# Kernel optimization log

Measured on AMD Instinct MI355X. Metric: run time of the kernel, lower is better.

Reference implementation:

```python
import jax, jax.numpy as jnp
import numpy as np

B, S, D, H = 16, 577, 1280, 16
HD = D // H  # 80
HALF = HD // 2  # 40


def setup_inputs() -> dict:
    key = jax.random.key(0)
    ks = jax.random.split(key, 8)
    hidden_states = jax.random.normal(ks[0], (B, S, D), dtype=jnp.float32)
    # 2D rotary frequencies: random angles -> unit-magnitude complex rotations
    angles = jax.random.uniform(ks[1], (S, HALF), dtype=jnp.float32) * (2.0 * np.pi)
    freqs_cos = jnp.cos(angles)
    freqs_sin = jnp.sin(angles)
    scale = 1.0 / np.sqrt(D)
    Wq = jax.random.normal(ks[2], (D, D), dtype=jnp.float32) * scale
    Wk = jax.random.normal(ks[3], (D, D), dtype=jnp.float32) * scale
    Wv = jax.random.normal(ks[4], (D, D), dtype=jnp.float32) * scale
    Wo = jax.random.normal(ks[5], (D, D), dtype=jnp.float32) * scale
    z = jnp.zeros((D,), dtype=jnp.float32)
    return {
        "hidden_states": hidden_states,
        "freqs_cos": freqs_cos,
        "freqs_sin": freqs_sin,
        "Wq": Wq, "bq": z, "Wk": Wk, "bk": z,
        "Wv": Wv, "bv": z, "Wo": Wo, "bo": z,
    }


def _apply_rotary(x, cos, sin):
    # x: [B,S,H,HD]; cos/sin: [S, HD/2]; interleaved complex pairs (even=real, odd=imag)
    xr = x[..., 0::2]
    xi = x[..., 1::2]
    c = cos[None, :, None, :]
    s = sin[None, :, None, :]
    out_r = xr * c - xi * s
    out_i = xr * s + xi * c
    # re-interleave pairs back to [..., HD]
    return jnp.stack([out_r, out_i], axis=-1).reshape(x.shape)


def reference(hidden_states, freqs_cos, freqs_sin, Wq, bq, Wk, bk, Wv, bv, Wo, bo):
    q = (hidden_states @ Wq.T + bq).reshape(B, S, H, HD)
    k = (hidden_states @ Wk.T + bk).reshape(B, S, H, HD)
    v = (hidden_states @ Wv.T + bv).reshape(B, S, H, HD)
    q = _apply_rotary(q, freqs_cos, freqs_sin)
    k = _apply_rotary(k, freqs_cos, freqs_sin)
    # [B,H,S,HD]
    q = q.transpose(0, 2, 1, 3)
    k = k.transpose(0, 2, 1, 3)
    v = v.transpose(0, 2, 1, 3)
    scale = 1.0 / np.sqrt(HD).astype(np.float32)
    scores = jnp.einsum("bhsd,bhtd->bhst", q, k) * scale
    probs = jax.nn.softmax(scores, axis=-1)
    attn = jnp.einsum("bhst,bhtd->bhsd", probs, v)
    attn = attn.transpose(0, 2, 1, 3).reshape(B, S, D)
    return attn @ Wo.T + bo
```

## Files before the change

### kernel.cpp

```cpp
#include <hip/hip_runtime.h>

#define B_N 16
#define S_N 577
#define D_N 1280
#define H_N 16
#define HD_N 80
#define HALF_N 40
#define M_N 9232
#define M_PAD 9344
#define K_N 1280
#define VT_S 608
#define QSCALE 0.11180339887498949f

typedef __bf16 bf16_t;
typedef bf16_t bf16x8 __attribute__((ext_vector_type(8)));
typedef float f32x4 __attribute__((ext_vector_type(4)));

__device__ __forceinline__ float bf2f(unsigned short u) {
    union { unsigned int i; float f; } x; x.i = ((unsigned int)u) << 16; return x.f;
}
__device__ __forceinline__ unsigned short f2bf(float f) {
    union { unsigned int i; float f; } x; x.f = f;
    unsigned int r = x.i + 0x7FFFu + ((x.i >> 16) & 1u);
    return (unsigned short)(r >> 16);
}

__device__ __forceinline__ void gld_lds16(const unsigned short* g, unsigned short* l) {
    __builtin_amdgcn_global_load_lds(
        (const __attribute__((address_space(1))) unsigned int*)g,
        (__attribute__((address_space(3))) unsigned int*)l,
        16, 0, 0);
}

__global__ __launch_bounds__(256) void cvt_kernel(const float* __restrict__ in,
                                                  unsigned short* __restrict__ out, int n4) {
    int i = blockIdx.x * 256 + threadIdx.x;
    if (i < n4) {
        float4 v = ((const float4*)in)[i];
        ushort4 o;
        o.x = f2bf(v.x); o.y = f2bf(v.y); o.z = f2bf(v.z); o.w = f2bf(v.w);
        ((ushort4*)out)[i] = o;
    }
}

#define W4_N (D_N * K_N / 4)
__global__ __launch_bounds__(256) void cvt4_kernel(
    const float* __restrict__ w0, const float* __restrict__ w1,
    const float* __restrict__ w2, const float* __restrict__ w3,
    unsigned short* __restrict__ out) {
    int i = blockIdx.x * 256 + threadIdx.x;
    if (i >= 4 * W4_N) return;
    int r = i / W4_N, j = i - r * W4_N;
    const float* src = (r == 0) ? w0 : (r == 1) ? w1 : (r == 2) ? w2 : w3;
    float4 v = ((const float4*)src)[j];
    ushort4 o;
    o.x = f2bf(v.x); o.y = f2bf(v.y); o.z = f2bf(v.z); o.w = f2bf(v.w);
    ((ushort4*)out)[i] = o;
}

__global__ __launch_bounds__(256) void qkv32_kernel(
    const unsigned short* __restrict__ A,
    const unsigned short* __restrict__ Wb,
    const float* __restrict__ b0, const float* __restrict__ b1,
    const float* __restrict__ b2,
    const float* __restrict__ cosb, const float* __restrict__ sinb,
    void* __restrict__ o0, void* __restrict__ o1, void* __restrict__ o2)
{
    __shared__ __align__(16) unsigned short As[4][128 * 32];
    __shared__ __align__(16) unsigned short Bs[4][128 * 32];

    const int tid = threadIdx.x;
    const int wave = tid >> 6, lane = tid & 63;
    const int quad = lane >> 4, n = lane & 15;
    const int wm = wave >> 1, wn = wave & 1;
    const int m0 = blockIdx.y * 128, n0g = blockIdx.x * 128;

    const int scb = (lane & 3) ^ ((lane >> 3) & 3);

    const unsigned short* gA = A + (size_t)(m0 + wave * 32 + (lane >> 2)) * K_N + scb * 8;
    const unsigned short* gB = Wb + (size_t)(n0g + wave * 32 + (lane >> 2)) * K_N + scb * 8;

    f32x4 acc[4][4] = {};

    auto stage = [&](int s, int kt) {
        unsigned short* lA = &As[s][wave * 1024];
        unsigned short* lB = &Bs[s][wave * 1024];
        const unsigned short* a = gA + kt * 32;
        const unsigned short* b = gB + kt * 32;
        gld_lds16(a, lA);
        gld_lds16(a + 16 * K_N, lA + 512);
        gld_lds16(b, lB);
        gld_lds16(b + 16 * K_N, lB + 512);
    };

    const int sa_blk = (quad ^ ((n >> 1) & 3)) * 8;
    auto compute = [&](int s) {
        bf16x8 af[4], bfr[4];
        #pragma unroll
        for (int nt = 0; nt < 4; ++nt)
            bfr[nt] = *(const bf16x8*)&Bs[s][(wn * 64 + nt * 16 + n) * 32 + sa_blk];
        #pragma unroll
        for (int mt = 0; mt < 4; ++mt)
            af[mt] = *(const bf16x8*)&As[s][(wm * 64 + mt * 16 + n) * 32 + sa_blk];
        #pragma unroll
        for (int mt = 0; mt < 4; ++mt)
            #pragma unroll
            for (int nt = 0; nt < 4; ++nt)
                acc[mt][nt] = __builtin_amdgcn_mfma_f32_16x16x32_bf16(
                    af[mt], bfr[nt], acc[mt][nt], 0, 0, 0);
    };

    stage(0, 0); stage(1, 1); stage(2, 2);

    #pragma unroll 4
    for (int t = 0; t < 40; ++t) {
        const int tn = (t + 3 < 40) ? t + 3 : 39;
        stage((t + 3) & 3, tn);
        asm volatile("s_waitcnt vmcnt(12)" ::: "memory");
        __builtin_amdgcn_s_barrier();
        compute(t & 3);
        __builtin_amdgcn_s_barrier();
    }
    asm volatile("s_waitcnt vmcnt(0)" ::: "memory");

    const int mbase = m0 + wm * 64;
    const int wsel = blockIdx.x / 10;
    const float* bias = (wsel == 0) ? b0 : (wsel == 1) ? b1 : b2;
    unsigned short* out =
        (unsigned short*)((wsel == 0) ? o0 : (wsel == 1) ? o1 : o2);
    const int nloc = n0g - wsel * 1280 + wn * 64;
    const bool evn = (n & 1) == 0;
    #pragma unroll
    for (int nt = 0; nt < 4; ++nt) {
        const int ncol = nloc + nt * 16 + n;
        const int h = ncol / HD_N, hd = ncol - h * HD_N;
        const float bv = bias[ncol];
        #pragma unroll
        for (int mt = 0; mt < 4; ++mt)
            #pragma unroll
            for (int r = 0; r < 4; ++r) {
                int mrow = mbase + mt * 16 + quad * 4 + r;
                int b = mrow / S_N, s = mrow - b * S_N;
                float v = acc[mt][nt][r] + bv;
                if (wsel == 2) {
                    if (mrow < M_N)
                        out[((size_t)(b * H_N + h) * HD_N + hd) * VT_S + s] = f2bf(v);
                } else {
                    float pv = __shfl_xor(v, 1);
                    float c  = cosb[s * HALF_N + (hd >> 1)];
                    float sn = sinb[s * HALF_N + (hd >> 1)];
                    float res = evn ? (v * c - pv * sn) : (pv * sn + v * c);
                    if (wsel == 0) res *= QSCALE;
                    if (mrow < M_N)
                        out[((size_t)(b * H_N + h) * S_N + s) * HD_N + hd] = f2bf(res);
                }
            }
    }
}

__global__ __launch_bounds__(256) void mgemm64_kernel(
    const unsigned short* __restrict__ A,
    const unsigned short* __restrict__ Wb,
    const float* __restrict__ b0,
    void* __restrict__ o0)
{
    __shared__ __align__(16) unsigned short As[2][128 * 64];
    __shared__ __align__(16) unsigned short Bs[2][128 * 64];

    const int tid = threadIdx.x;
    const int wave = tid >> 6, lane = tid & 63;
    const int quad = lane >> 4, n = lane & 15;
    const int wm = wave >> 1, wn = wave & 1;
    const int m0 = blockIdx.y * 128, n0g = blockIdx.x * 128;

    const int srow = lane >> 3;
    const int scol = (((lane & 7) ^ srow) * 8);

    const unsigned short* gA = A + (size_t)(m0 + wave * 32 + srow) * K_N + scol;
    const unsigned short* gB = Wb + (size_t)(n0g + wave * 32 + srow) * K_N + scol;
    const int lofs = wave * 32 * 64;

    f32x4 acc[4][4] = {};

    auto stage = [&](int pp, int k0) {
        unsigned short* lA = &As[pp][lofs];
        unsigned short* lB = &Bs[pp][lofs];
        #pragma unroll
        for (int i = 0; i < 4; ++i) {
            gld_lds16(gA + k0 + i * 8 * K_N, lA + i * 512);
            gld_lds16(gB + k0 + i * 8 * K_N, lB + i * 512);
        }
    };

    auto compute = [&](int pp) {
        #pragma unroll
        for (int kk = 0; kk < 2; ++kk) {
            const int sa = ((((kk << 2) | quad) ^ (n & 7)) * 8);
            bf16x8 af[4], bfr[4];
            #pragma unroll
            for (int mt = 0; mt < 4; ++mt)
                af[mt] = *(const bf16x8*)&As[pp][(wm * 64 + mt * 16 + n) * 64 + sa];
            #pragma unroll
            for (int nt = 0; nt < 4; ++nt)
                bfr[nt] = *(const bf16x8*)&Bs[pp][(wn * 64 + nt * 16 + n) * 64 + sa];
            #pragma unroll
            for (int mt = 0; mt < 4; ++mt)
                #pragma unroll
                for (int nt = 0; nt < 4; ++nt)
                    acc[mt][nt] = __builtin_amdgcn_mfma_f32_16x16x32_bf16(
                        af[mt], bfr[nt], acc[mt][nt], 0, 0, 0);
        }
    };

    stage(0, 0);

    #pragma unroll 2
    for (int t = 0; t < 19; ++t) {
        const int pp = t & 1;
        stage(pp ^ 1, (t + 1) * 64);
        asm volatile("s_waitcnt vmcnt(8)" ::: "memory");
        __builtin_amdgcn_s_barrier();
        compute(pp);
        __builtin_amdgcn_s_barrier();
    }
    asm volatile("s_waitcnt vmcnt(0)" ::: "memory");
    __builtin_amdgcn_s_barrier();
    compute(1);

    const int mbase = m0 + wm * 64;
    const int nbase = n0g + wn * 64;
    float* outp = (float*)o0;
    #pragma unroll
    for (int mt = 0; mt < 4; ++mt)
        #pragma unroll
        for (int nt = 0; nt < 4; ++nt) {
            const int ncol = nbase + nt * 16 + n;
            const float bv = b0[ncol];
            #pragma unroll
            for (int r = 0; r < 4; ++r) {
                int mrow = mbase + mt * 16 + quad * 4 + r;
                if (mrow < M_N)
                    outp[(size_t)mrow * D_N + ncol] = acc[mt][nt][r] + bv;
            }
        }
}

__global__ __launch_bounds__(256) void fattn_kernel(
    const unsigned short* __restrict__ qb,
    const unsigned short* __restrict__ kb,
    const unsigned short* __restrict__ vt,
    unsigned short* __restrict__ attn)
{
    __shared__ __align__(16) unsigned short Plds[4][2][2][16 * 32];

    const int tid = threadIdx.x;
    const int wave = tid >> 6, lane = tid & 63;
    const int quad = lane >> 4, n = lane & 15;

    const int bid = blockIdx.x;
    const int xcd = bid & 7, t = bid >> 3;
    const int qt = t % 5, hl = t / 5;
    const int bh = hl * 8 + xcd;
    const int q0 = qt * 128 + wave * 32;

    const bf16x8 zf{};
    const unsigned short* qrow0 = qb + ((size_t)bh * S_N + q0 + n) * HD_N;
    const unsigned short* qrow1 = qrow0 + 16 * HD_N;
    bf16x8 aq00 = *(const bf16x8*)(qrow0 + quad * 8);
    bf16x8 aq01 = *(const bf16x8*)(qrow0 + 32 + quad * 8);
    bf16x8 aq02 = (quad < 2) ? *(const bf16x8*)(qrow0 + 64 + quad * 8) : zf;
    bf16x8 aq10 = *(const bf16x8*)(qrow1 + quad * 8);
    bf16x8 aq11 = *(const bf16x8*)(qrow1 + 32 + quad * 8);
    bf16x8 aq12 = (quad < 2) ? *(const bf16x8*)(qrow1 + 64 + quad * 8) : zf;

    const bf16_t one = (bf16_t)1.0f;
    const bf16x8 vones_all = {one, one, one, one, one, one, one, one};
    const bf16x8 vones = (n == 0) ? vones_all : zf;

    f32x4 o0[6] = {};
    f32x4 o1[6] = {};

    const unsigned short* kbase = kb + (size_t)bh * S_N * HD_N;
    const unsigned short* vbase = vt + (size_t)bh * HD_N * VT_S;

    #pragma unroll 2
    for (int t0 = 0; t0 < 608; t0 += 32) {
        const int pp = (t0 >> 5) & 1;
        unsigned short* pl0 = &Plds[wave][pp][0][0];
        unsigned short* pl1 = &Plds[wave][pp][1][0];

        const unsigned short* krA = kbase + (size_t)(t0 + n) * HD_N;
        const unsigned short* krB = krA + 16 * HD_N;
        bf16x8 bA0 = *(const bf16x8*)(krA + quad * 8);
        bf16x8 bA1 = *(const bf16x8*)(krA + 32 + quad * 8);
        bf16x8 bA2 = (quad < 2) ? *(const bf16x8*)(krA + 64 + quad * 8) : zf;
        bf16x8 bB0 = *(const bf16x8*)(krB + quad * 8);
        bf16x8 bB1 = *(const bf16x8*)(krB + 32 + quad * 8);
        bf16x8 bB2 = (quad < 2) ? *(const bf16x8*)(krB + 64 + quad * 8) : zf;

        f32x4 c00{}, c01{}, c10{}, c11{};
        c00 = __builtin_amdgcn_mfma_f32_16x16x32_bf16(aq00, bA0, c00, 0, 0, 0);
        c00 = __builtin_amdgcn_mfma_f32_16x16x32_bf16(aq01, bA1, c00, 0, 0, 0);
        c00 = __builtin_amdgcn_mfma_f32_16x16x32_bf16(aq02, bA2, c00, 0, 0, 0);
        c01 = __builtin_amdgcn_mfma_f32_16x16x32_bf16(aq00, bB0, c01, 0, 0, 0);
        c01 = __builtin_amdgcn_mfma_f32_16x16x32_bf16(aq01, bB1, c01, 0, 0, 0);
        c01 = __builtin_amdgcn_mfma_f32_16x16x32_bf16(aq02, bB2, c01, 0, 0, 0);
        c10 = __builtin_amdgcn_mfma_f32_16x16x32_bf16(aq10, bA0, c10, 0, 0, 0);
        c10 = __builtin_amdgcn_mfma_f32_16x16x32_bf16(aq11, bA1, c10, 0, 0, 0);
        c10 = __builtin_amdgcn_mfma_f32_16x16x32_bf16(aq12, bA2, c10, 0, 0, 0);
        c11 = __builtin_amdgcn_mfma_f32_16x16x32_bf16(aq10, bB0, c11, 0, 0, 0);
        c11 = __builtin_amdgcn_mfma_f32_16x16x32_bf16(aq11, bB1, c11, 0, 0, 0);
        c11 = __builtin_amdgcn_mfma_f32_16x16x32_bf16(aq12, bB2, c11, 0, 0, 0);

        const bool mA = (t0 + n) >= S_N;
        const bool mB = (t0 + 16 + n) >= S_N;

        #pragma unroll
        for (int r = 0; r < 4; ++r) {
            float p00 = mA ? 0.0f : __expf(c00[r]);
            float p01 = mB ? 0.0f : __expf(c01[r]);
            float p10 = mA ? 0.0f : __expf(c10[r]);
            float p11 = mB ? 0.0f : __expf(c11[r]);
            pl0[(quad * 4 + r) * 32 + n]      = f2bf(p00);
            pl0[(quad * 4 + r) * 32 + 16 + n] = f2bf(p01);
            pl1[(quad * 4 + r) * 32 + n]      = f2bf(p10);
            pl1[(quad * 4 + r) * 32 + 16 + n] = f2bf(p11);
        }

        bf16x8 ap0 = *(const bf16x8*)(pl0 + n * 32 + quad * 8);
        bf16x8 ap1 = *(const bf16x8*)(pl1 + n * 32 + quad * 8);

        #pragma unroll
        for (int nt = 0; nt < 5; ++nt) {
            const unsigned short* vr = vbase + (size_t)(nt * 16 + n) * VT_S + t0 + quad * 8;
            bf16x8 bv = *(const bf16x8*)vr;
            o0[nt] = __builtin_amdgcn_mfma_f32_16x16x32_bf16(ap0, bv, o0[nt], 0, 0, 0);
            o1[nt] = __builtin_amdgcn_mfma_f32_16x16x32_bf16(ap1, bv, o1[nt], 0, 0, 0);
        }
        o0[5] = __builtin_amdgcn_mfma_f32_16x16x32_bf16(ap0, vones, o0[5], 0, 0, 0);
        o1[5] = __builtin_amdgcn_mfma_f32_16x16x32_bf16(ap1, vones, o1[5], 0, 0, 0);
    }

    const int b = bh >> 4, h = bh & 15;
    #pragma unroll
    for (int r = 0; r < 4; ++r) {
        float l0 = __shfl(o0[5][r], lane & 48);
        float l1 = __shfl(o1[5][r], lane & 48);
        float linv0 = 1.0f / l0, linv1 = 1.0f / l1;
        int s0 = q0 + quad * 4 + r;
        int s1 = s0 + 16;
        #pragma unroll
        for (int nt = 0; nt < 5; ++nt) {
            if (s0 < S_N)
                attn[((size_t)b * S_N + s0) * D_N + h * HD_N + nt * 16 + n] =
                    f2bf(o0[nt][r] * linv0);
            if (s1 < S_N)
                attn[((size_t)b * S_N + s1) * D_N + h * HD_N + nt * 16 + n] =
                    f2bf(o1[nt][r] * linv1);
        }
    }
}

extern "C" void kernel_launch(void* const* d_in, const int* in_sizes, int n_in,
                              void* d_out, int out_size, void* d_ws, size_t ws_size,
                              hipStream_t stream) {
    const float* hs = (const float*)d_in[0];
    const float* fc = (const float*)d_in[1];
    const float* fs = (const float*)d_in[2];
    const float* Wq = (const float*)d_in[3];
    const float* bq = (const float*)d_in[4];
    const float* Wk = (const float*)d_in[5];
    const float* bk = (const float*)d_in[6];
    const float* Wv = (const float*)d_in[7];
    const float* bv = (const float*)d_in[8];
    const float* Wo = (const float*)d_in[9];
    const float* bo = (const float*)d_in[10];
    float* out = (float*)d_out;

    char* ws = (char*)d_ws;
    size_t off = 0;
    auto alloc = [&](size_t bytes) {
        char* p = ws + off; off += (bytes + 255) & ~(size_t)255; return p;
    };
    unsigned short* hsb  = (unsigned short*)alloc((size_t)M_PAD * K_N * 2);
    unsigned short* qb   = (unsigned short*)alloc((size_t)M_N * K_N * 2 + 32768);
    unsigned short* kb   = (unsigned short*)alloc((size_t)M_N * K_N * 2 + 32768);
    unsigned short* vt   = (unsigned short*)alloc((size_t)B_N * H_N * HD_N * VT_S * 2);
    unsigned short* Wall = (unsigned short*)alloc((size_t)4 * D_N * K_N * 2);

    const int HS4 = M_N * K_N / 4;
    dim3 blk(256);

    cvt_kernel<<<(HS4 + 255) / 256, blk, 0, stream>>>(hs, hsb, HS4);
    cvt4_kernel<<<(4 * W4_N + 255) / 256, blk, 0, stream>>>(Wq, Wk, Wv, Wo, Wall);

    qkv32_kernel<<<dim3(30, 73), blk, 0, stream>>>(
        hsb, Wall, bq, bk, bv, fc, fs, qb, kb, vt);

    fattn_kernel<<<dim3(1280), blk, 0, stream>>>(qb, kb, vt, hsb );

    mgemm64_kernel<<<dim3(10, 73), blk, 0, stream>>>(
        hsb, Wall + 3 * (size_t)D_N * K_N, bo, out);
}
```

Before: 479.7 us.

## Restructure QKV GEMM to 8 waves with BK=64 double-buffered LDS pipeline

The fused QKV projection kernel now runs with 512 threads (8 waves in a 2x4 grid) instead of 4 waves. Each wave computes a 64x32 sub-tile instead of 64x64. The K-step grows from 32 to 64 with a two-stage LDS buffer in place of the four-stage ring, and the XOR swizzle is adjusted for 64-wide rows. The intent is more waves to hide latency and fewer barriers per K. In exchange, each wave does fewer MFMAs per LDS fragment load and the prefetch depth is shallower.

```diff
diff --git a/kernel.cpp b/kernel.cpp
--- a/kernel.cpp
+++ b/kernel.cpp
@@ -58,7 +58,7 @@
     ((ushort4*)out)[i] = o;
 }
 
-__global__ __launch_bounds__(256) void qkv32_kernel(
+__global__ __launch_bounds__(512) void qkv8w_kernel(
     const unsigned short* __restrict__ A,
     const unsigned short* __restrict__ Wb,
     const float* __restrict__ b0, const float* __restrict__ b1,
@@ -66,82 +66,88 @@
     const float* __restrict__ cosb, const float* __restrict__ sinb,
     void* __restrict__ o0, void* __restrict__ o1, void* __restrict__ o2)
 {
-    __shared__ __align__(16) unsigned short As[4][128 * 32];
-    __shared__ __align__(16) unsigned short Bs[4][128 * 32];
+    __shared__ __align__(16) unsigned short As[2][128 * 64];
+    __shared__ __align__(16) unsigned short Bs[2][128 * 64];
 
     const int tid = threadIdx.x;
     const int wave = tid >> 6, lane = tid & 63;
     const int quad = lane >> 4, n = lane & 15;
-    const int wm = wave >> 1, wn = wave & 1;
+    const int wm = wave >> 2, wn = wave & 3;
     const int m0 = blockIdx.y * 128, n0g = blockIdx.x * 128;
 
-    const int scb = (lane & 3) ^ ((lane >> 3) & 3);
-
-    const unsigned short* gA = A + (size_t)(m0 + wave * 32 + (lane >> 2)) * K_N + scb * 8;
-    const unsigned short* gB = Wb + (size_t)(n0g + wave * 32 + (lane >> 2)) * K_N + scb * 8;
-
-    f32x4 acc[4][4] = {};
+    const int srow = tid >> 3;
+    const int scb  = (tid & 7) ^ (srow & 7);
+
+    const unsigned short* gA = A + (size_t)(m0 + srow) * K_N + scb * 8;
+    const unsigned short* gB = Wb + (size_t)(n0g + srow) * K_N + scb * 8;
+    const int lofs = wave * 512;
+
+    f32x4 acc[4][2] = {};
 
     auto stage = [&](int s, int kt) {
-        unsigned short* lA = &As[s][wave * 1024];
-        unsigned short* lB = &Bs[s][wave * 1024];
-        const unsigned short* a = gA + kt * 32;
-        const unsigned short* b = gB + kt * 32;
-        gld_lds16(a, lA);
-        gld_lds16(a + 16 * K_N, lA + 512);
-        gld_lds16(b, lB);
-        gld_lds16(b + 16 * K_N, lB + 512);
+        const unsigned short* a = gA + kt * 64;
+        const unsigned short* b = gB + kt * 64;
+        gld_lds16(a, &As[s][lofs]);
+        gld_lds16(a + (size_t)64 * K_N, &As[s][lofs + 4096]);
+        gld_lds16(b, &Bs[s][lofs]);
+        gld_lds16(b + (size_t)64 * K_N, &Bs[s][lofs + 4096]);
     };
 
-    const int sa_blk = (quad ^ ((n >> 1) & 3)) * 8;
     auto compute = [&](int s) {
-        bf16x8 af[4], bfr[4];
-        #pragma unroll
-        for (int nt = 0; nt < 4; ++nt)
-            bfr[nt] = *(const bf16x8*)&Bs[s][(wn * 64 + nt * 16 + n) * 32 + sa_blk];
-        #pragma unroll
-        for (int mt = 0; mt < 4; ++mt)
-            af[mt] = *(const bf16x8*)&As[s][(wm * 64 + mt * 16 + n) * 32 + sa_blk];
-        #pragma unroll
-        for (int mt = 0; mt < 4; ++mt)
-            #pragma unroll
-            for (int nt = 0; nt < 4; ++nt)
-                acc[mt][nt] = __builtin_amdgcn_mfma_f32_16x16x32_bf16(
-                    af[mt], bfr[nt], acc[mt][nt], 0, 0, 0);
+        #pragma unroll
+        for (int kk = 0; kk < 2; ++kk) {
+            const int sa = ((((kk << 2) | quad) ^ (n & 7)) * 8);
+            bf16x8 af[4], bfr[2];
+            #pragma unroll
+            for (int nf = 0; nf < 2; ++nf)
+                bfr[nf] = *(const bf16x8*)&Bs[s][(wn * 32 + nf * 16 + n) * 64 + sa];
+            #pragma unroll
+            for (int mf = 0; mf < 4; ++mf)
+                af[mf] = *(const bf16x8*)&As[s][(wm * 64 + mf * 16 + n) * 64 + sa];
+            #pragma unroll
+            for (int mf = 0; mf < 4; ++mf)
+                #pragma unroll
+                for (int nf = 0; nf < 2; ++nf)
+                    acc[mf][nf] = __builtin_amdgcn_mfma_f32_16x16x32_bf16(
+                        af[mf], bfr[nf], acc[mf][nf], 0, 0, 0);
+        }
     };
 
-    stage(0, 0); stage(1, 1); stage(2, 2);
-
-    #pragma unroll 4
-    for (int t = 0; t < 40; ++t) {
-        const int tn = (t + 3 < 40) ? t + 3 : 39;
-        stage((t + 3) & 3, tn);
-        asm volatile("s_waitcnt vmcnt(12)" ::: "memory");
+    stage(0, 0);
+
+    #pragma unroll 2
+    for (int t = 0; t < 19; ++t) {
+        const int s = t & 1;
+        stage(s ^ 1, t + 1);
+        asm volatile("s_waitcnt vmcnt(4)" ::: "memory");
         __builtin_amdgcn_s_barrier();
-        compute(t & 3);
+        compute(s);
         __builtin_amdgcn_s_barrier();
     }
     asm volatile("s_waitcnt vmcnt(0)" ::: "memory");
-
-    const int mbase = m0 + wm * 64;
+    __builtin_amdgcn_s_barrier();
+    compute(1);
+
     const int wsel = blockIdx.x / 10;
     const float* bias = (wsel == 0) ? b0 : (wsel == 1) ? b1 : b2;
     unsigned short* out =
         (unsigned short*)((wsel == 0) ? o0 : (wsel == 1) ? o1 : o2);
-    const int nloc = n0g - wsel * 1280 + wn * 64;
+    const int nloc = n0g - wsel * 1280 + wn * 32;
+    const int mbase = m0 + wm * 64;
     const bool evn = (n & 1) == 0;
+
     #pragma unroll
-    for (int nt = 0; nt < 4; ++nt) {
-        const int ncol = nloc + nt * 16 + n;
+    for (int nf = 0; nf < 2; ++nf) {
+        const int ncol = nloc + nf * 16 + n;
         const int h = ncol / HD_N, hd = ncol - h * HD_N;
         const float bv = bias[ncol];
         #pragma unroll
-        for (int mt = 0; mt < 4; ++mt)
+        for (int mf = 0; mf < 4; ++mf)
             #pragma unroll
             for (int r = 0; r < 4; ++r) {
-                int mrow = mbase + mt * 16 + quad * 4 + r;
+                int mrow = mbase + mf * 16 + quad * 4 + r;
                 int b = mrow / S_N, s = mrow - b * S_N;
-                float v = acc[mt][nt][r] + bv;
+                float v = acc[mf][nf][r] + bv;
                 if (wsel == 2) {
                     if (mrow < M_N)
                         out[((size_t)(b * H_N + h) * HD_N + hd) * VT_S + s] = f2bf(v);
@@ -394,7 +400,7 @@
     cvt_kernel<<<(HS4 + 255) / 256, blk, 0, stream>>>(hs, hsb, HS4);
     cvt4_kernel<<<(4 * W4_N + 255) / 256, blk, 0, stream>>>(Wq, Wk, Wv, Wo, Wall);
 
-    qkv32_kernel<<<dim3(30, 73), blk, 0, stream>>>(
+    qkv8w_kernel<<<dim3(30, 73), dim3(512), 0, stream>>>(
         hsb, Wall, bq, bk, bv, fc, fs, qb, kb, vt);
 
     fattn_kernel<<<dim3(1280), blk, 0, stream>>>(qb, kb, vt, hsb );
```

Result: faster. 419.2 us (-12.6%).
